# Performance work log

Measured on AMD Instinct MI355X. Metric: run time of the kernel, lower is better.

The kernel has to match this reference:

```python
import jax, jax.numpy as jnp
import numpy as np

E, H_HEADS, WS = 512, 16, 8
HEAD_D = E // H_HEADS
LN_EPS = 1e-5


def layernorm(x, g, b):
    mu = jnp.mean(x, axis=-1, keepdims=True)
    var = jnp.mean((x - mu) ** 2, axis=-1, keepdims=True)
    return (x - mu) / jnp.sqrt(var + LN_EPS) * g + b


def setup_inputs() -> dict:
    key = jax.random.key(0)
    ks = jax.random.split(key, 10)
    s = 0.02
    return {
        "x": jax.random.normal(ks[0], (4, 4096, E), jnp.float32),
        "in_proj_w": jax.random.normal(ks[1], (3 * E, E), jnp.float32) * s,
        "in_proj_b": jnp.zeros((3 * E,), jnp.float32),
        "out_w": jax.random.normal(ks[2], (E, E), jnp.float32) * s,
        "out_b": jnp.zeros((E,), jnp.float32),
        "ln1_g": jnp.ones((E,), jnp.float32),
        "ln1_b": jnp.zeros((E,), jnp.float32),
        "w1": jax.random.normal(ks[3], (4 * E, E), jnp.float32) * s,
        "b1": jnp.zeros((4 * E,), jnp.float32),
        "w2": jax.random.normal(ks[4], (E, 4 * E), jnp.float32) * s,
        "b2": jnp.zeros((E,), jnp.float32),
        "ln2_g": jnp.ones((E,), jnp.float32),
        "ln2_b": jnp.zeros((E,), jnp.float32),
        "num_patches_h": 64,
        "num_patches_w": 64,
    }


def reference(x, in_proj_w, in_proj_b, out_w, out_b, ln1_g, ln1_b,
              w1, b1, w2, b2, ln2_g, ln2_b, num_patches_h, num_patches_w):
    B, P, _ = x.shape
    Hp, Wp = num_patches_h, num_patches_w  # 64 divisible by WS -> no padding branch
    nwh, nww = Hp // WS, Wp // WS
    # window partition: (B, Hp, Wp, E) -> (B*nW, WS*WS, E)
    xw = x.reshape(B, nwh, WS, nww, WS, E).transpose(0, 1, 3, 2, 4, 5)
    xw = xw.reshape(B * nwh * nww, WS * WS, E)
    # nn.MultiheadAttention default batch_first=False: axis0 is SEQ (L=B*nW),
    # axis1 is BATCH (N=WS*WS). Reproduce that literal semantics.
    L, N = xw.shape[0], xw.shape[1]
    qkv = xw @ in_proj_w.T + in_proj_b          # (L, N, 3E)
    q, k, v = jnp.split(qkv, 3, axis=-1)
    qh = q.reshape(L, N, H_HEADS, HEAD_D)
    kh = k.reshape(L, N, H_HEADS, HEAD_D)
    vh = v.reshape(L, N, H_HEADS, HEAD_D)
    scale = 1.0 / np.sqrt(HEAD_D)
    scores = jnp.einsum('lnhd,mnhd->nhlm', qh, kh) * scale  # (N, h, L, L)
    attn = jax.nn.softmax(scores, axis=-1)
    o = jnp.einsum('nhlm,mnhd->lnhd', attn, vh).reshape(L, N, E)
    attn_out = o @ out_w.T + out_b
    y = layernorm(xw + attn_out, ln1_g, ln1_b)
    ffn = jax.nn.gelu(y @ w1.T + b1, approximate=False) @ w2.T + b2
    y = layernorm(y + ffn, ln2_g, ln2_b)
    # window unpartition
    y = y.reshape(B, nwh, nww, WS, WS, E).transpose(0, 1, 3, 2, 4, 5)
    return y.reshape(B, Hp * Wp, E)[:, :P, :]
```

## Files before the change

kernel.cpp:

```cpp
#include <hip/hip_runtime.h>
#include <cmath>


typedef _Float16 half8 __attribute__((ext_vector_type(8)));
typedef _Float16 half4v __attribute__((ext_vector_type(4)));
typedef float f32x4 __attribute__((ext_vector_type(4)));

#define GLOBAL_AS(p) ((const __attribute__((address_space(1))) void*)(p))
#define LDS_AS(p) ((__attribute__((address_space(3))) void*)(p))

__device__ __forceinline__ void gload_lds16(const _Float16* g, _Float16* l) {
  __builtin_amdgcn_global_load_lds(GLOBAL_AS(g), LDS_AS(l), 16, 0, 0);
}

__device__ __forceinline__ float wave_sum(float v) {
#pragma unroll
  for (int off = 32; off > 0; off >>= 1) v += __shfl_xor(v, off, 64);
  return v;
}

__device__ __forceinline__ float gelu_fast(float x) {
  const float y = 1.5957691216057308f * (x + 0.044715f * x * x * x);
  const float e = __expf(y);
  const float t = 1.0f - 2.0f / (e + 1.0f);
  return 0.5f * x * (1.0f + t);
}

__global__ __launch_bounds__(256) void pre_kernel(
    const float* __restrict__ x, _Float16* __restrict__ xw,
    const float* __restrict__ s0, _Float16* __restrict__ d0,
    const float* __restrict__ s1, _Float16* __restrict__ d1,
    const float* __restrict__ s2, _Float16* __restrict__ d2,
    const float* __restrict__ s3, _Float16* __restrict__ d3) {
  int b = blockIdx.x;
  if (b < 4096) {
    const int idx = b * 256 + threadIdx.x;
    const int t = idx >> 6;
    const int e0 = (idx & 63) << 3;
    const int l = t >> 6, n = t & 63;
    const int bb = l >> 6, wh = (l >> 3) & 7, ww = l & 7;
    const int pi = n >> 3, pj = n & 7;
    const int xrow = (bb * 4096 + (wh * 8 + pi) * 64 + (ww * 8 + pj)) * 512;
    const float4 a = *(const float4*)&x[xrow + e0];
    const float4 c = *(const float4*)&x[xrow + e0 + 4];
    half8 o;
    o[0] = (_Float16)a.x; o[1] = (_Float16)a.y; o[2] = (_Float16)a.z; o[3] = (_Float16)a.w;
    o[4] = (_Float16)c.x; o[5] = (_Float16)c.y; o[6] = (_Float16)c.z; o[7] = (_Float16)c.w;
    *(half8*)&xw[t * 512 + e0] = o;
    return;
  }
  b -= 4096;
  const float* s; _Float16* d;
  if (b < 768) { s = s0; d = d0; }
  else if (b < 1024) { s = s1; d = d1; b -= 768; }
  else if (b < 2048) { s = s2; d = d2; b -= 1024; }
  else { s = s3; d = d3; b -= 2048; }
  const int i = (b * 256 + threadIdx.x) * 4;
  const float4 v = *(const float4*)&s[i];
  half4v o;
  o[0] = (_Float16)v.x; o[1] = (_Float16)v.y; o[2] = (_Float16)v.z; o[3] = (_Float16)v.w;
  *(half4v*)&d[i] = o;
}

template <int EPI, int K, int BN>
__global__ __launch_bounds__(256, 4) void gemml_kernel(
    const _Float16* __restrict__ A, const _Float16* __restrict__ B,
    const float* __restrict__ bias, _Float16* __restrict__ C, int N) {
  constexpr int NT = K / 64;
  constexpr int TA = 128 * 64;
  constexpr int TB = BN * 64;
  constexpr int MREP = (BN == 128) ? 4 : 2;
  __shared__ _Float16 L[TA + TB];

  const int tid = threadIdx.x, lane = tid & 63, wave = tid >> 6;
  const int wr = (BN == 128) ? (wave >> 1) : wave;
  const int wc = (BN == 128) ? (wave & 1) : 0;
  const int lr = lane & 15, g = lane >> 4;

  const int nbn = N / BN;
  const int cpx = gridDim.x >> 3;
  const int wg = (blockIdx.x & 7) * cpx + (blockIdx.x >> 3);
  const int bm = wg / nbn, bn = wg % nbn;

  const int scol = ((lane & 7) ^ (lane >> 3)) << 3;
  const int srow = lane >> 3;
  const _Float16* aS = A + (size_t)(bm * 128 + wave * 8 + srow) * K + scol;
  const _Float16* bS = B + (size_t)(bn * BN + wave * 8 + srow) * K + scol;

  const int sw0 = ((g ^ (lr & 7)) << 3);
  const int sw1 = (((4 + g) ^ (lr & 7)) << 3);
  int arow[MREP], brow[4];
#pragma unroll
  for (int m = 0; m < MREP; ++m) arow[m] = (wr * (MREP * 16) + m * 16 + lr) * 64;
#pragma unroll
  for (int n = 0; n < 4; ++n) brow[n] = TA + (wc * 64 + n * 16 + lr) * 64;

  f32x4 acc[MREP][4] = {};

#pragma unroll 8
  for (int t = 0; t < NT; ++t) {
    const int koff = t * 64;
#pragma unroll
    for (int i = 0; i < 4; ++i)
      gload_lds16(aS + (size_t)(i * 32) * K + koff, &L[(i * 32 + wave * 8) * 64]);
#pragma unroll
    for (int i = 0; i < BN / 32; ++i)
      gload_lds16(bS + (size_t)(i * 32) * K + koff, &L[TA + (i * 32 + wave * 8) * 64]);
    __syncthreads();
    half8 af[MREP], bf[4];
#pragma unroll
    for (int m = 0; m < MREP; ++m) af[m] = *(const half8*)&L[arow[m] + sw0];
#pragma unroll
    for (int n = 0; n < 4; ++n) bf[n] = *(const half8*)&L[brow[n] + sw0];
    __builtin_amdgcn_s_setprio(1);
#pragma unroll
    for (int m = 0; m < MREP; ++m)
#pragma unroll
      for (int n = 0; n < 4; ++n)
        acc[m][n] = __builtin_amdgcn_mfma_f32_16x16x32_f16(af[m], bf[n], acc[m][n], 0, 0, 0);
    __builtin_amdgcn_s_setprio(0);
#pragma unroll
    for (int m = 0; m < MREP; ++m) af[m] = *(const half8*)&L[arow[m] + sw1];
#pragma unroll
    for (int n = 0; n < 4; ++n) bf[n] = *(const half8*)&L[brow[n] + sw1];
    __builtin_amdgcn_s_setprio(1);
#pragma unroll
    for (int m = 0; m < MREP; ++m)
#pragma unroll
      for (int n = 0; n < 4; ++n)
        acc[m][n] = __builtin_amdgcn_mfma_f32_16x16x32_f16(af[m], bf[n], acc[m][n], 0, 0, 0);
    __builtin_amdgcn_s_setprio(0);
    __syncthreads();
  }

  float bsv[4];
#pragma unroll
  for (int n = 0; n < 4; ++n) bsv[n] = bias[bn * BN + wc * 64 + n * 16 + lr];
  _Float16* Lc = &L[0] + wave * (MREP * 16 * 64);
#pragma unroll
  for (int m = 0; m < MREP; ++m)
#pragma unroll
    for (int n = 0; n < 4; ++n)
#pragma unroll
      for (int r = 0; r < 4; ++r) {
        float v = acc[m][n][r] + bsv[n];
        if (EPI == 1) v = gelu_fast(v);
        const int row = m * 16 + g * 4 + r;
        const int col = n * 16 + lr;
        Lc[row * 64 + (col ^ ((row & 7) << 3))] = (_Float16)v;
      }
  asm volatile("s_waitcnt lgkmcnt(0)" ::: "memory");
  const int rrow = lane >> 3, slot = lane & 7;
  const int growb = bm * 128 + wr * (MREP * 16);
  const int gcol = bn * BN + wc * 64 + slot * 8;
#pragma unroll
  for (int blk = 0; blk < MREP * 2; ++blk) {
    const int row = blk * 8 + rrow;
    const half8 vv = *(const half8*)&Lc[row * 64 + ((slot ^ (row & 7)) << 3)];
    *(half8*)&C[(size_t)(growb + row) * N + gcol] = vv;
  }
}

__global__ __launch_bounds__(256) void attn_kernel(const _Float16* __restrict__ qkv,
                                                   _Float16* __restrict__ o_out) {
  const int n = blockIdx.x & 63;
  const int h = blockIdx.x >> 6;
  __shared__ _Float16 Ksh[256 * 40];
  __shared__ _Float16 Vt[32 * 264];
  __shared__ _Float16 Pw[4 * 64 * 72];
  const int tid = threadIdx.x;
  const int wq = tid >> 6, lane = tid & 63;
  const int lr = lane & 15, g = lane >> 4;
  const int hq = h * 32;

#pragma unroll
  for (int pass = 0; pass < 4; ++pass) {
    const int e = pass * 2048 + tid * 8;
    const int m = e >> 5, d = e & 31;
    const int base = (m * 64 + n) * 1536 + hq;
    const half8 k8 = *(const half8*)&qkv[base + 512 + d];
    const half8 v8 = *(const half8*)&qkv[base + 1024 + d];
    *(half8*)&Ksh[m * 40 + d] = k8;
#pragma unroll
    for (int j = 0; j < 8; ++j) Vt[(d + j) * 264 + m] = v8[j];
  }
  half8 qf[4];
#pragma unroll
  for (int qt = 0; qt < 4; ++qt) {
    const int qg = wq * 64 + qt * 16 + lr;
    qf[qt] = *(const half8*)&qkv[(qg * 64 + n) * 1536 + hq + g * 8];
  }
  __syncthreads();

  f32x4 o[4][2] = {};
  float den[4] = {0.f, 0.f, 0.f, 0.f};
  const float scale = 0.17677669529663687f;
  _Float16* P = &Pw[wq * (64 * 72)];

  for (int it = 0; it < 4; ++it) {
    const int k0 = it * 64;
#pragma unroll
    for (int qt = 0; qt < 4; ++qt) {
#pragma unroll
      for (int kt = 0; kt < 4; ++kt) {
        const half8 kf = *(const half8*)&Ksh[(k0 + kt * 16 + lr) * 40 + g * 8];
        const f32x4 z = {0.f, 0.f, 0.f, 0.f};
        f32x4 st = __builtin_amdgcn_mfma_f32_16x16x32_f16(kf, qf[qt], z, 0, 0, 0);
        const float p0 = __expf(st[0] * scale);
        const float p1 = __expf(st[1] * scale);
        const float p2 = __expf(st[2] * scale);
        const float p3 = __expf(st[3] * scale);
        den[qt] += (p0 + p1) + (p2 + p3);
        half4v w;
        w[0] = (_Float16)p0; w[1] = (_Float16)p1;
        w[2] = (_Float16)p2; w[3] = (_Float16)p3;
        *(half4v*)&P[(qt * 16 + lr) * 72 + kt * 16 + g * 4] = w;
      }
    }
    __syncthreads();
#pragma unroll
    for (int qt = 0; qt < 4; ++qt) {
#pragma unroll
      for (int ks = 0; ks < 2; ++ks) {
        const half8 pf = *(const half8*)&P[(qt * 16 + lr) * 72 + ks * 32 + g * 8];
#pragma unroll
        for (int dt = 0; dt < 2; ++dt) {
          const half8 vf = *(const half8*)&Vt[(dt * 16 + lr) * 264 + k0 + ks * 32 + g * 8];
          o[qt][dt] = __builtin_amdgcn_mfma_f32_16x16x32_f16(pf, vf, o[qt][dt], 0, 0, 0);
        }
      }
    }
    __syncthreads();
  }

#pragma unroll
  for (int qt = 0; qt < 4; ++qt) {
    float dq = den[qt];
    dq += __shfl_xor(dq, 16);
    dq += __shfl_xor(dq, 32);
    const float inv = 1.0f / dq;
#pragma unroll
    for (int r = 0; r < 4; ++r) {
      const float invr = __shfl(inv, g * 4 + r);
      const int qg = wq * 64 + qt * 16 + g * 4 + r;
      const int obase = (qg * 64 + n) * 512 + hq;
#pragma unroll
      for (int dt = 0; dt < 2; ++dt)
        o_out[obase + dt * 16 + lr] = (_Float16)(o[qt][dt][r] * invr);
    }
  }
}

template <int FINAL>
__global__ __launch_bounds__(256) void ln_kernel(
    const float* __restrict__ res32, const _Float16* __restrict__ res16,
    const _Float16* __restrict__ add16,
    const float* __restrict__ g, const float* __restrict__ b,
    float* __restrict__ out32, _Float16* __restrict__ out16) {
  const int t = blockIdx.x * 4 + (threadIdx.x >> 6);
  const int lane = threadIdx.x & 63;
  const int e0 = lane << 3;
  const int l = t >> 6, n = t & 63;
  const int bb = l >> 6, wh = (l >> 3) & 7, ww = l & 7;
  const int pi = n >> 3, pj = n & 7;
  const int xrow = (bb * 4096 + (wh * 8 + pi) * 64 + (ww * 8 + pj)) * 512;
  const int trow = t * 512;
  const half8 a8 = *(const half8*)&add16[trow + e0];
  float v[8];
  if (FINAL) {
    const half8 r8 = *(const half8*)&res16[trow + e0];
#pragma unroll
    for (int e = 0; e < 8; ++e) v[e] = (float)r8[e] + (float)a8[e];
  } else {
    const float4 ra = *(const float4*)&res32[xrow + e0];
    const float4 rb = *(const float4*)&res32[xrow + e0 + 4];
    v[0] = ra.x + (float)a8[0]; v[1] = ra.y + (float)a8[1];
    v[2] = ra.z + (float)a8[2]; v[3] = ra.w + (float)a8[3];
    v[4] = rb.x + (float)a8[4]; v[5] = rb.y + (float)a8[5];
    v[6] = rb.z + (float)a8[6]; v[7] = rb.w + (float)a8[7];
  }
  float sm = 0.f;
#pragma unroll
  for (int e = 0; e < 8; ++e) sm += v[e];
  sm = wave_sum(sm);
  const float mu = sm * (1.0f / 512.0f);
  float vs = 0.f;
#pragma unroll
  for (int e = 0; e < 8; ++e) { const float d = v[e] - mu; vs += d * d; }
  vs = wave_sum(vs);
  const float rstd = rsqrtf(vs * (1.0f / 512.0f) + 1e-5f);
  const float4 g1 = *(const float4*)&g[e0];
  const float4 g2 = *(const float4*)&g[e0 + 4];
  const float4 b1 = *(const float4*)&b[e0];
  const float4 b2 = *(const float4*)&b[e0 + 4];
  float y[8];
  y[0] = (v[0] - mu) * rstd * g1.x + b1.x; y[1] = (v[1] - mu) * rstd * g1.y + b1.y;
  y[2] = (v[2] - mu) * rstd * g1.z + b1.z; y[3] = (v[3] - mu) * rstd * g1.w + b1.w;
  y[4] = (v[4] - mu) * rstd * g2.x + b2.x; y[5] = (v[5] - mu) * rstd * g2.y + b2.y;
  y[6] = (v[6] - mu) * rstd * g2.z + b2.z; y[7] = (v[7] - mu) * rstd * g2.w + b2.w;
  if (FINAL) {
    *(float4*)&out32[xrow + e0] = make_float4(y[0], y[1], y[2], y[3]);
    *(float4*)&out32[xrow + e0 + 4] = make_float4(y[4], y[5], y[6], y[7]);
  } else {
    half8 o16;
#pragma unroll
    for (int e = 0; e < 8; ++e) o16[e] = (_Float16)y[e];
    *(half8*)&out16[trow + e0] = o16;
  }
}

extern "C" void kernel_launch(void* const* d_in, const int* in_sizes, int n_in,
                              void* d_out, int out_size, void* d_ws, size_t ws_size,
                              hipStream_t stream) {
  const float* x    = (const float*)d_in[0];
  const float* ipw  = (const float*)d_in[1];
  const float* ipb  = (const float*)d_in[2];
  const float* outw = (const float*)d_in[3];
  const float* outb = (const float*)d_in[4];
  const float* ln1g = (const float*)d_in[5];
  const float* ln1b = (const float*)d_in[6];
  const float* w1   = (const float*)d_in[7];
  const float* b1   = (const float*)d_in[8];
  const float* w2   = (const float*)d_in[9];
  const float* b2   = (const float*)d_in[10];
  const float* ln2g = (const float*)d_in[11];
  const float* ln2b = (const float*)d_in[12];
  float* out = (float*)d_out;
  char* ws = (char*)d_ws;

  _Float16* wqkv_h = (_Float16*)(ws + 0);
  _Float16* wout_h = (_Float16*)(ws + 1572864);
  _Float16* w1_h   = (_Float16*)(ws + 2097152);
  _Float16* w2_h   = (_Float16*)(ws + 4194304);
  _Float16* xw_h   = (_Float16*)(ws + 6291456);
  _Float16* qkv_h  = (_Float16*)(ws + 23068672);
  _Float16* attn_h = (_Float16*)(ws + 90177536);
  _Float16* ao_h   = (_Float16*)(ws + 106954752);
  _Float16* h_h = qkv_h;
  _Float16* f_h = attn_h;
  _Float16* y16 = xw_h;

  pre_kernel<<<7168, 256, 0, stream>>>(x, xw_h, ipw, wqkv_h, outw, wout_h,
                                       w1, w1_h, w2, w2_h);
  gemml_kernel<0, 512, 128><<<1536, 256, 0, stream>>>(xw_h, wqkv_h, ipb, qkv_h, 1536);
  attn_kernel<<<1024, 256, 0, stream>>>(qkv_h, attn_h);
  gemml_kernel<0, 512, 64><<<1024, 256, 0, stream>>>(attn_h, wout_h, outb, ao_h, 512);
  ln_kernel<0><<<4096, 256, 0, stream>>>(x, nullptr, ao_h, ln1g, ln1b, nullptr, y16);
  gemml_kernel<1, 512, 128><<<2048, 256, 0, stream>>>(y16, w1_h, b1, h_h, 2048);
  gemml_kernel<0, 2048, 64><<<1024, 256, 0, stream>>>(h_h, w2_h, b2, f_h, 512);
  ln_kernel<1><<<4096, 256, 0, stream>>>(nullptr, y16, f_h, ln2g, ln2b, out, nullptr);
}
```

Before: 203.2 us.

## Add 256x256-tile 8-wave ping-pong GEMM for QKV and FFN1 projections

Adds a new GEMM kernel that uses 256x256 output tiles with 512 threads (8 waves). It double-buffers LDS through direct global-to-LDS loads, splits each K-tile into phases with barriers and raised wave priority around the MFMA blocks, and writes output through a swizzled LDS staging pass. The QKV and FFN-up GEMMs now use it instead of the 128-row tiled kernel, which raises data reuse per loaded byte and overlaps loads with matrix math. The cost is fewer workgroups (384/512), which risks a wave-quantization tail on 256 CUs, plus heavier register and LDS use that limits occupancy.

```diff
diff --git a/kernel.cpp b/kernel.cpp
--- a/kernel.cpp
+++ b/kernel.cpp
@@ -62,6 +62,124 @@
   *(half4v*)&d[i] = o;
 }
 
+#define MFMA16(MH)                                                          \
+  _Pragma("unroll") for (int m = 0; m < 4; ++m)                             \
+  _Pragma("unroll") for (int n = 0; n < 4; ++n)                             \
+    acc[(MH)*4+m][n] = __builtin_amdgcn_mfma_f32_16x16x32_f16(af[m], bf[n], acc[(MH)*4+m][n], 0, 0, 0);
+
+#define G201_PHASE(BUFI, MH, KK, STAGE, GATE)                               \
+  {                                                                         \
+    const _Float16* Ar = &L[BUFI][(KK) * HALF];                             \
+    const _Float16* Br = &L[BUFI][(2 + (KK)) * HALF];                       \
+    half8 af[4], bf[4];                                                     \
+    _Pragma("unroll") for (int m = 0; m < 4; ++m)                           \
+      af[m] = *(const half8*)&Ar[arow[(MH)*4+m]];                           \
+    _Pragma("unroll") for (int n = 0; n < 4; ++n)                           \
+      bf[n] = *(const half8*)&Br[brow[n]];                                  \
+    STAGE;                                                                  \
+    asm volatile("s_barrier" ::: "memory");                                 \
+    asm volatile("s_waitcnt lgkmcnt(0)" ::: "memory");                      \
+    __builtin_amdgcn_sched_barrier(0);                                      \
+    __builtin_amdgcn_s_setprio(1);                                          \
+    MFMA16(MH);                                                             \
+    __builtin_amdgcn_s_setprio(0);                                         \
+    if (GATE) asm volatile("s_waitcnt vmcnt(8)" ::: "memory");              \
+    asm volatile("s_barrier" ::: "memory");                                 \
+  }
+
+template <int EPI, int K>
+__global__ __launch_bounds__(512, 2) void g201_kernel(
+    const _Float16* __restrict__ A, const _Float16* __restrict__ B,
+    const float* __restrict__ bias, _Float16* __restrict__ C, int N) {
+  constexpr int NT = K / 64;
+  constexpr int NI = NT / 2;
+  constexpr int HALF = 256 * 32;
+  __shared__ _Float16 L[2][4 * HALF];
+
+  const int tid = threadIdx.x, lane = tid & 63, wave = tid >> 6;
+  const int wr = wave >> 2, wc = wave & 3;
+  const int lr = lane & 15, g = lane >> 4;
+
+  const int nbn = N >> 8;
+  const int cpx = gridDim.x >> 3;
+  const int wg = (blockIdx.x & 7) * cpx + (blockIdx.x >> 3);
+  const int bm = wg / nbn, bn = wg % nbn;
+
+  const int srow = lane >> 2;
+  const int scol = (((lane & 3) ^ ((lane >> 3) & 3)) << 3);
+  const _Float16* aG = A + (size_t)(bm * 256 + wave * 16 + srow) * K + scol;
+  const _Float16* bG = B + (size_t)(bn * 256 + wave * 16 + srow) * K + scol;
+
+#define STAGE_A(BUFI, TT, KK)                                               \
+  { _Float16* dst = &L[BUFI][(KK) * HALF + wave * 16 * 32];                 \
+    const _Float16* src = aG + (TT) * 64 + (KK) * 32;                       \
+    gload_lds16(src, dst);                                                  \
+    gload_lds16(src + (size_t)128 * K, dst + 128 * 32); }
+#define STAGE_B(BUFI, TT, KK)                                               \
+  { _Float16* dst = &L[BUFI][(2 + (KK)) * HALF + wave * 16 * 32];           \
+    const _Float16* src = bG + (TT) * 64 + (KK) * 32;                       \
+    gload_lds16(src, dst);                                                  \
+    gload_lds16(src + (size_t)128 * K, dst + 128 * 32); }
+
+  const int sw = ((g ^ ((lr >> 1) & 3)) << 3);
+  int arow[8], brow[4];
+#pragma unroll
+  for (int m = 0; m < 8; ++m) arow[m] = (wr * 128 + m * 16 + lr) * 32 + sw;
+#pragma unroll
+  for (int n = 0; n < 4; ++n) brow[n] = (wc * 64 + n * 16 + lr) * 32 + sw;
+
+  f32x4 acc[8][4] = {};
+
+  STAGE_A(0, 0, 0); STAGE_B(0, 0, 0);
+  STAGE_A(0, 0, 1); STAGE_B(0, 0, 1);
+  STAGE_A(1, 1, 0); STAGE_B(1, 1, 0);
+  asm volatile("s_waitcnt vmcnt(8)" ::: "memory");
+  asm volatile("s_barrier" ::: "memory");
+
+#pragma unroll 2
+  for (int i = 0; i < NI; ++i) {
+    const int T1 = 2 * i + 1, E = 2 * i + 2, F = 2 * i + 3;
+    G201_PHASE(0, 0, 0, STAGE_A(1, T1, 1), false);
+    G201_PHASE(0, 1, 0, STAGE_B(1, T1, 1), true);
+    G201_PHASE(0, 0, 1, if (E < NT) STAGE_A(0, E, 0), false);
+    G201_PHASE(0, 1, 1, if (E < NT) STAGE_B(0, E, 0), true);
+    G201_PHASE(1, 0, 0, if (E < NT) STAGE_A(0, E, 1), false);
+    G201_PHASE(1, 1, 0, if (E < NT) STAGE_B(0, E, 1), true);
+    G201_PHASE(1, 0, 1, if (F < NT) STAGE_A(1, F, 0), false);
+    G201_PHASE(1, 1, 1, if (F < NT) STAGE_B(1, F, 0), true);
+  }
+  asm volatile("s_waitcnt vmcnt(0) lgkmcnt(0)" ::: "memory");
+  asm volatile("s_barrier" ::: "memory");
+
+  float bsv[4];
+#pragma unroll
+  for (int n = 0; n < 4; ++n) bsv[n] = bias[bn * 256 + wc * 64 + n * 16 + lr];
+  _Float16* Lc = &L[0][0] + wave * 8192;
+#pragma unroll
+  for (int m = 0; m < 8; ++m)
+#pragma unroll
+    for (int n = 0; n < 4; ++n)
+#pragma unroll
+      for (int r = 0; r < 4; ++r) {
+        float v = acc[m][n][r] + bsv[n];
+        if (EPI == 1) v = gelu_fast(v);
+        const int row = m * 16 + g * 4 + r;
+        const int col = n * 16 + lr;
+        Lc[row * 64 + (col ^ ((row & 7) << 3))] = (_Float16)v;
+      }
+  asm volatile("s_waitcnt lgkmcnt(0)" ::: "memory");
+  __syncthreads();
+  const int rrow = lane >> 3, slot = lane & 7;
+  const int grow = bm * 256 + wr * 128;
+  const int gcol = bn * 256 + wc * 64 + slot * 8;
+#pragma unroll
+  for (int blk = 0; blk < 16; ++blk) {
+    const int row = blk * 8 + rrow;
+    const half8 vv = *(const half8*)&Lc[row * 64 + ((slot ^ (row & 7)) << 3)];
+    *(half8*)&C[(size_t)(grow + row) * N + gcol] = vv;
+  }
+}
+
 template <int EPI, int K, int BN>
 __global__ __launch_bounds__(256, 4) void gemml_kernel(
     const _Float16* __restrict__ A, const _Float16* __restrict__ B,
@@ -342,11 +460,11 @@
 
   pre_kernel<<<7168, 256, 0, stream>>>(x, xw_h, ipw, wqkv_h, outw, wout_h,
                                        w1, w1_h, w2, w2_h);
-  gemml_kernel<0, 512, 128><<<1536, 256, 0, stream>>>(xw_h, wqkv_h, ipb, qkv_h, 1536);
+  g201_kernel<0, 512><<<384, 512, 0, stream>>>(xw_h, wqkv_h, ipb, qkv_h, 1536);
   attn_kernel<<<1024, 256, 0, stream>>>(qkv_h, attn_h);
   gemml_kernel<0, 512, 64><<<1024, 256, 0, stream>>>(attn_h, wout_h, outb, ao_h, 512);
   ln_kernel<0><<<4096, 256, 0, stream>>>(x, nullptr, ao_h, ln1g, ln1b, nullptr, y16);
-  gemml_kernel<1, 512, 128><<<2048, 256, 0, stream>>>(y16, w1_h, b1, h_h, 2048);
+  g201_kernel<1, 512><<<512, 512, 0, stream>>>(y16, w1_h, b1, h_h, 2048);
   gemml_kernel<0, 2048, 64><<<1024, 256, 0, stream>>>(h_h, w2_h, b2, f_h, 512);
   ln_kernel<1><<<4096, 256, 0, stream>>>(nullptr, y16, f_h, ln2g, ln2b, out, nullptr);
 }
```

Result: slower. 235.8 us (+16.1%).
